# Kernel tuning notes

Hardware: AMD Instinct MI355X
Metric: run time of the kernel (lower is better)

Reference implementation:

```python
import jax, jax.numpy as jnp
import numpy as np

B, N, D = 2, 2048, 1024   # batch, seq_len, d_model
E = 2 * D                  # d_inner = d_model * expand_factor
F = 4 * D                  # ffn hidden
CHUNK = 128
EPS_LN = 1e-5


def setup_inputs() -> dict:
    key = jax.random.key(0)
    ks = jax.random.split(key, 16)
    s = 0.02
    return {
        "x": jax.random.normal(ks[0], (B, N, D), dtype=jnp.float32),
        # linear-attention projections (stored [in, out])
        "q_w": jax.random.normal(ks[1], (D, E), dtype=jnp.float32) * s,
        "q_b": jnp.zeros((E,), jnp.float32),
        "k_w": jax.random.normal(ks[2], (D, E), dtype=jnp.float32) * s,
        "k_b": jnp.zeros((E,), jnp.float32),
        "v_w": jax.random.normal(ks[3], (D, E), dtype=jnp.float32) * s,
        "v_b": jnp.zeros((E,), jnp.float32),
        "o_w": jax.random.normal(ks[4], (E, D), dtype=jnp.float32) * s,
        "o_b": jnp.zeros((D,), jnp.float32),
        # layer norms
        "ln1_g": jnp.ones((D,), jnp.float32), "ln1_b": jnp.zeros((D,), jnp.float32),
        "ln2_g": jnp.ones((D,), jnp.float32), "ln2_b": jnp.zeros((D,), jnp.float32),
        # ffn
        "w1": jax.random.normal(ks[5], (D, F), dtype=jnp.float32) * s,
        "b1": jnp.zeros((F,), jnp.float32),
        "w2": jax.random.normal(ks[6], (F, D), dtype=jnp.float32) * s,
        "b2": jnp.zeros((D,), jnp.float32),
    }


def _layer_norm(x, g, b):
    mu = jnp.mean(x, axis=-1, keepdims=True)
    var = jnp.mean(jnp.square(x - mu), axis=-1, keepdims=True)
    return (x - mu) * jax.lax.rsqrt(var + EPS_LN) * g + b


def _feature_map(x):
    return jax.nn.elu(x) + 1.0  # positive features


def _causal_linear_attention(Q, K, V):
    """Exactly cumsum(k v^T) formulation, computed chunk-recurrently.
    Q,K: [B,N,E] (post feature map), V: [B,N,E]. Returns [B,N,E]."""
    nC = N // CHUNK
    Qc = Q.reshape(B, nC, CHUNK, E).transpose(1, 0, 2, 3)
    Kc = K.reshape(B, nC, CHUNK, E).transpose(1, 0, 2, 3)
    Vc = V.reshape(B, nC, CHUNK, E).transpose(1, 0, 2, 3)
    tril = jnp.tril(jnp.ones((CHUNK, CHUNK), Q.dtype))

    def step(S, qkv):  # S: [B,E,E] running sum of k v^T
        q, k, v = qkv
        scores = jnp.einsum('bcd,bkd->bck', q, k) * tril  # intra-chunk causal
        intra = jnp.einsum('bck,bke->bce', scores, v)
        inter = jnp.einsum('bcd,bde->bce', q, S)
        S = S + jnp.einsum('bcd,bce->bde', k, v)
        return S, intra + inter

    S0 = jnp.zeros((B, E, E), Q.dtype)
    _, num = jax.lax.scan(step, S0, (Qc, Kc, Vc))  # [nC,B,CHUNK,E]
    num = num.transpose(1, 0, 2, 3).reshape(B, N, E)
    Z = jnp.cumsum(K, axis=1)                       # [B,N,E]
    den = jnp.einsum('bnd,bnd->bn', Q, Z)[..., None] + 1e-6
    return num / den


def reference(x, q_w, q_b, k_w, k_b, v_w, v_b, o_w, o_b,
              ln1_g, ln1_b, ln2_g, ln2_b, w1, b1, w2, b2):
    # training branch of SSDFLUIDLayer (linear attention), dropout = identity (eval)
    xn = _layer_norm(x, ln1_g, ln1_b)
    Q = _feature_map(xn @ q_w + q_b)
    K = _feature_map(xn @ k_w + k_b)
    V = xn @ v_w + v_b
    attn = _causal_linear_attention(Q, K, V) @ o_w + o_b
    x = x + attn
    xn2 = _layer_norm(x, ln2_g, ln2_b)
    ffn = jax.nn.gelu(xn2 @ w1 + b1, approximate=False) @ w2 + b2
    return x + ffn
```

## Files before the change

### kernel.cpp

```cpp
#include <hip/hip_runtime.h>
#include <math.h>

typedef unsigned short u16;
typedef short s16x8 __attribute__((ext_vector_type(8)));
typedef float f32x4 __attribute__((ext_vector_type(4)));
typedef long long ll;

__device__ inline u16 f2bf(float f) {
    unsigned u = __float_as_uint(f);
    u += 0x7fffu + ((u >> 16) & 1u);
    return (u16)(u >> 16);
}
__device__ inline float bf2f(u16 h) { return __uint_as_float(((unsigned)h) << 16); }

__device__ __forceinline__ void glds16(const u16* g, u16* l) {
    __builtin_amdgcn_global_load_lds(
        (__attribute__((address_space(1))) void*)(void*)g,
        (__attribute__((address_space(3))) void*)l, 16, 0, 0);
}

__global__ __launch_bounds__(256) void ln_bf16(const float* __restrict__ x,
                                               const float* __restrict__ g,
                                               const float* __restrict__ b,
                                               u16* __restrict__ out, int D) {
    int row = blockIdx.x;
    const float* xr = x + (size_t)row * D;
    int t = threadIdx.x;
    float4 v = ((const float4*)xr)[t];
    float s = v.x + v.y + v.z + v.w;
    __shared__ float sm[4];
    #pragma unroll
    for (int o = 32; o > 0; o >>= 1) s += __shfl_down(s, o, 64);
    int lane = t & 63, wv = t >> 6;
    if (lane == 0) sm[wv] = s;
    __syncthreads();
    float mean = (sm[0] + sm[1] + sm[2] + sm[3]) * (1.0f / 1024.0f);
    float dx = v.x - mean, dy = v.y - mean, dz = v.z - mean, dw = v.w - mean;
    float s2 = dx * dx + dy * dy + dz * dz + dw * dw;
    __syncthreads();
    #pragma unroll
    for (int o = 32; o > 0; o >>= 1) s2 += __shfl_down(s2, o, 64);
    if (lane == 0) sm[wv] = s2;
    __syncthreads();
    float var = (sm[0] + sm[1] + sm[2] + sm[3]) * (1.0f / 1024.0f);
    float rstd = rsqrtf(var + 1e-5f);
    float4 gg = ((const float4*)g)[t], bb = ((const float4*)b)[t];
    ushort4 o4;
    o4.x = f2bf(dx * rstd * gg.x + bb.x);
    o4.y = f2bf(dy * rstd * gg.y + bb.y);
    o4.z = f2bf(dz * rstd * gg.z + bb.z);
    o4.w = f2bf(dw * rstd * gg.w + bb.w);
    ((ushort4*)(out + (size_t)row * D))[t] = o4;
}

__global__ __launch_bounds__(256) void combine_ln(
    const float* __restrict__ x, const float* __restrict__ p0,
    const float* __restrict__ p1, const float* __restrict__ ob,
    const float* __restrict__ g, const float* __restrict__ b,
    float* __restrict__ x2, u16* __restrict__ xn2) {
    int row = blockIdx.x;
    int t = threadIdx.x;
    size_t base = (size_t)row * 256;
    float4 v = ((const float4*)x)[base + t];
    float4 a0 = ((const float4*)p0)[base + t];
    float4 a1 = ((const float4*)p1)[base + t];
    float4 ob4 = ((const float4*)ob)[t];
    v.x += a0.x + a1.x + ob4.x;
    v.y += a0.y + a1.y + ob4.y;
    v.z += a0.z + a1.z + ob4.z;
    v.w += a0.w + a1.w + ob4.w;
    ((float4*)x2)[base + t] = v;
    float s = v.x + v.y + v.z + v.w;
    __shared__ float sm[4];
    #pragma unroll
    for (int o = 32; o > 0; o >>= 1) s += __shfl_down(s, o, 64);
    int lane = t & 63, wv = t >> 6;
    if (lane == 0) sm[wv] = s;
    __syncthreads();
    float mean = (sm[0] + sm[1] + sm[2] + sm[3]) * (1.0f / 1024.0f);
    float dx = v.x - mean, dy = v.y - mean, dz = v.z - mean, dw = v.w - mean;
    float s2 = dx * dx + dy * dy + dz * dz + dw * dw;
    __syncthreads();
    #pragma unroll
    for (int o = 32; o > 0; o >>= 1) s2 += __shfl_down(s2, o, 64);
    if (lane == 0) sm[wv] = s2;
    __syncthreads();
    float var = (sm[0] + sm[1] + sm[2] + sm[3]) * (1.0f / 1024.0f);
    float rstd = rsqrtf(var + 1e-5f);
    float4 gg = ((const float4*)g)[t], bb = ((const float4*)b)[t];
    ushort4 o4;
    o4.x = f2bf(dx * rstd * gg.x + bb.x);
    o4.y = f2bf(dy * rstd * gg.y + bb.y);
    o4.z = f2bf(dz * rstd * gg.z + bb.z);
    o4.w = f2bf(dw * rstd * gg.w + bb.w);
    ((ushort4*)(xn2 + (size_t)row * 1024))[t] = o4;
}

__global__ __launch_bounds__(256) void combine_out(
    const float* __restrict__ x2, const float* __restrict__ p0,
    const float* __restrict__ p1, const float* __restrict__ b2,
    float* __restrict__ out) {
    size_t i = (size_t)blockIdx.x * 256 + threadIdx.x;
    int col4 = (int)(i & 255);
    float4 v = ((const float4*)x2)[i];
    float4 a0 = ((const float4*)p0)[i];
    float4 a1 = ((const float4*)p1)[i];
    float4 bb = ((const float4*)b2)[col4];
    v.x += a0.x + a1.x + bb.x;
    v.y += a0.y + a1.y + bb.y;
    v.z += a0.z + a1.z + bb.z;
    v.w += a0.w + a1.w + bb.w;
    ((float4*)out)[i] = v;
}

__global__ void prep(const float* __restrict__ qb, const float* __restrict__ kb,
                     const float* __restrict__ vb, float* __restrict__ bcat,
                     float* __restrict__ den, int E, int BN) {
    int i = blockIdx.x * 256 + threadIdx.x;
    if (i < E) {
        bcat[i] = qb[i];
        bcat[E + i] = kb[i];
        bcat[2 * E + i] = vb[i];
    }
    if (i < BN) den[i] = 0.f;
}

__global__ __launch_bounds__(256) void transpose_all(
    const float* __restrict__ q_w, const float* __restrict__ k_w,
    const float* __restrict__ v_w, const float* __restrict__ o_w,
    const float* __restrict__ w1, const float* __restrict__ w2,
    u16* __restrict__ qkvT, u16* __restrict__ oT,
    u16* __restrict__ w1T, u16* __restrict__ w2T) {
    int z = blockIdx.y;
    const float* src;
    u16* dst;
    int R, C, tprLog;
    switch (z) {
        case 0: src = q_w; dst = qkvT;                           R = 1024; C = 2048; tprLog = 6; break;
        case 1: src = k_w; dst = qkvT + (size_t)2 * 1024 * 1024; R = 1024; C = 2048; tprLog = 6; break;
        case 2: src = v_w; dst = qkvT + (size_t)4 * 1024 * 1024; R = 1024; C = 2048; tprLog = 6; break;
        case 3: src = o_w; dst = oT;                             R = 2048; C = 1024; tprLog = 5; break;
        case 4: src = w1;  dst = w1T;                            R = 1024; C = 4096; tprLog = 7; break;
        default: src = w2; dst = w2T;                            R = 4096; C = 1024; tprLog = 5; break;
    }
    int bx = blockIdx.x;
    int ntiles = (R >> 5) << (tprLog);
    if (bx >= ntiles) return;
    int c0 = (bx & ((1 << tprLog) - 1)) * 32;
    int r0 = (bx >> tprLog) * 32;
    __shared__ u16 tile[32][33];
    int tx = threadIdx.x & 31, ty = threadIdx.x >> 5;
    #pragma unroll
    for (int i = 0; i < 32; i += 8)
        tile[ty + i][tx] = f2bf(src[(size_t)(r0 + ty + i) * C + c0 + tx]);
    __syncthreads();
    #pragma unroll
    for (int i = 0; i < 32; i += 8)
        dst[(size_t)(c0 + ty + i) * R + r0 + tx] = tile[tx][ty + i];
}

__global__ __launch_bounds__(256) void transpose_u16(const u16* __restrict__ in,
                                                     u16* __restrict__ out,
                                                     int R, int C, int ldIn,
                                                     ll sIn, ll sOut) {
    in += (size_t)blockIdx.z * sIn;
    out += (size_t)blockIdx.z * sOut;
    __shared__ u16 tile[32][33];
    int tx = threadIdx.x & 31, ty = threadIdx.x >> 5;
    int c0 = blockIdx.x * 32, r0 = blockIdx.y * 32;
    #pragma unroll
    for (int i = 0; i < 32; i += 8)
        tile[ty + i][tx] = in[(size_t)(r0 + ty + i) * ldIn + c0 + tx];
    __syncthreads();
    #pragma unroll
    for (int i = 0; i < 32; i += 8)
        out[(size_t)(c0 + ty + i) * R + r0 + tx] = tile[tx][ty + i];
}

enum { EPI_QKV = 0, EPI_TRIL = 2, EPI_DIV = 3, EPI_GELU = 5, EPI_PART = 6 };

template <int EPI, int TNt>
__global__ __launch_bounds__(256, 2) void gemm2b(
    const u16* __restrict__ A, const u16* __restrict__ B, void* __restrict__ Cv,
    const float* __restrict__ bias, float* __restrict__ den,
    int M, int N, int K, int lda, int ldb,
    ll sA, ll sB, ll sC, ll sAux) {

    constexpr int NJ = TNt / 32;
    constexpr int BUF = 4096 + TNt * 32;
    __shared__ __align__(16) u16 lds[3][BUF];

    int z = blockIdx.z;
    A += (size_t)z * sA;
    B += (size_t)z * sB;

    int p = blockIdx.y * gridDim.x + blockIdx.x;
    int m0, n0;
    if (EPI == EPI_TRIL || EPI == EPI_DIV) {
        int nb = gridDim.x;
        int panel = nb * 4;
        int pp = p / panel, rr2 = p - pp * panel;
        m0 = (pp * 4 + (rr2 & 3)) * 128;
        n0 = (rr2 >> 2) * TNt;
    } else {
        int g = p & 7, rr2 = p >> 3;
        int lw = gridDim.x >> 2, lh = gridDim.y >> 1;
        int ly = rr2 / lw, lx = rr2 - ly * lw;
        m0 = ((g >> 2) * lh + ly) * 128;
        n0 = ((g & 3) * lw + lx) * TNt;
    }

    int t = threadIdx.x;

    if (EPI == EPI_TRIL && n0 > m0 + 127) {
        u16* C = (u16*)Cv + (size_t)z * sC;
        #pragma unroll
        for (int s = 0; s < 8; ++s) {
            int v = t + 256 * s;
            int row = v >> 4, cf = (v & 15) * 8;
            *(uint4*)&C[(size_t)(m0 + row) * N + n0 + cf] = make_uint4(0, 0, 0, 0);
        }
        return;
    }

    int lane = t & 63, wid = t >> 6;
    int lr = lane & 15, q = lane >> 4;

    int skf = (((lane & 3) - ((lane >> 3) & 3)) & 3) * 8;
    const u16* gA = A + (size_t)(m0 + wid * 32 + (lane >> 2)) * lda + skf;
    const u16* gB = B + (size_t)(n0 + wid * (TNt / 4) + (lane >> 2)) * ldb + skf;
    int sdA = wid * 1024;
    int sdB = 4096 + wid * (TNt * 32 / 4);

    int kend = (EPI == EPI_DIV) ? (m0 + 128 < K ? m0 + 128 : K) : K;
    int nk = kend >> 5;

    auto stageA = [&](int tt, int d) {
        int kt = (tt < nk ? tt : nk - 1) << 5;
        glds16(gA + kt, &lds[d][sdA]);
        glds16(gA + kt + (size_t)16 * lda, &lds[d][sdA + 512]);
    };
    auto stageB = [&](int tt, int d) {
        int kt = (tt < nk ? tt : nk - 1) << 5;
        #pragma unroll
        for (int r2 = 0; r2 < TNt / 64; ++r2)
            glds16(gB + kt + (size_t)(16 * r2) * ldb, &lds[d][sdB + r2 * 512]);
    };

    f32x4 acc[4][NJ];
    #pragma unroll
    for (int i = 0; i < 4; i++)
        #pragma unroll
        for (int j = 0; j < NJ; j++) { f32x4 zz = {0.f, 0.f, 0.f, 0.f}; acc[i][j] = zz; }

    int wm = (wid & 1) * 64, wn = (wid >> 1) * (TNt / 2);
    int csw = ((q + (lr >> 1)) & 3) * 8;
    int aoff = (wm + lr) * 32 + csw;
    int boff = 4096 + (wn + lr) * 32 + csw;

    stageA(0, 0); stageB(0, 0);
    stageA(1, 1); stageB(1, 1);
    if constexpr (TNt == 256) asm volatile("s_waitcnt vmcnt(6)" ::: "memory");
    else                      asm volatile("s_waitcnt vmcnt(4)" ::: "memory");
    asm volatile("s_barrier" ::: "memory");

    s16x8 af[4], bf_[NJ];

    int cur = 0;
    for (int tt = 0; tt < nk; ++tt) {
        int nx2 = cur + 2; if (nx2 >= 3) nx2 -= 3;
        const u16* L = &lds[cur][0];

        #pragma unroll
        for (int j = 0; j < NJ / 2; j++) bf_[j] = *(const s16x8*)&L[boff + j * 512];
        #pragma unroll
        for (int i = 0; i < 4; i++) af[i] = *(const s16x8*)&L[aoff + i * 512];
        stageB(tt + 2, nx2);
        asm volatile("s_barrier" ::: "memory");
        __builtin_amdgcn_s_setprio(1);
        #pragma unroll
        for (int i = 0; i < 4; i++)
            #pragma unroll
            for (int j = 0; j < NJ / 2; j++)
                acc[i][j] = __builtin_amdgcn_mfma_f32_16x16x32_bf16(af[i], bf_[j], acc[i][j], 0, 0, 0);
        __builtin_amdgcn_s_setprio(0);
        asm volatile("s_barrier" ::: "memory");

        #pragma unroll
        for (int j = NJ / 2; j < NJ; j++) bf_[j] = *(const s16x8*)&L[boff + j * 512];
        stageA(tt + 2, nx2);
        asm volatile("s_barrier" ::: "memory");
        __builtin_amdgcn_s_setprio(1);
        #pragma unroll
        for (int i = 0; i < 4; i++)
            #pragma unroll
            for (int j = NJ / 2; j < NJ; j++)
                acc[i][j] = __builtin_amdgcn_mfma_f32_16x16x32_bf16(af[i], bf_[j], acc[i][j], 0, 0, 0);
        __builtin_amdgcn_s_setprio(0);
        if constexpr (TNt == 256) asm volatile("s_waitcnt vmcnt(6)" ::: "memory");
        else                      asm volatile("s_waitcnt vmcnt(4)" ::: "memory");
        asm volatile("s_barrier" ::: "memory");

        cur = cur + 1; if (cur >= 3) cur -= 3;
    }

    asm volatile("s_waitcnt vmcnt(0)" ::: "memory");

    u16* Cb = (u16*)Cv + (size_t)z * ((EPI == EPI_PART) ? 0 : sC);
    float* Cf = (float*)Cv + (size_t)z * ((EPI == EPI_PART) ? sC : 0);
    bool isQKcol = (EPI == EPI_QKV);
    #pragma unroll
    for (int i = 0; i < 4; i++) {
        #pragma unroll
        for (int r = 0; r < 4; r++) {
            int row = m0 + wm + i * 16 + q * 4 + r;
            float rs = 0.f;
            #pragma unroll
            for (int j = 0; j < NJ; j++) {
                int col = n0 + wn + j * 16 + lr;
                float v = acc[i][j][r];
                if (EPI == EPI_PART) {
                    Cf[(size_t)row * N + col] = v;
                } else if (EPI == EPI_TRIL) {
                    v = (col <= row) ? v : 0.f;
                    rs += v;
                    Cb[(size_t)row * N + col] = f2bf(v);
                } else if (EPI == EPI_DIV) {
                    float d = den[(size_t)z * sAux + row] + 1e-6f;
                    Cb[(size_t)row * N + col] = f2bf(v / d);
                } else {
                    v += bias[col];
                    if (EPI == EPI_QKV) {
                        if (isQKcol && (n0 + wn + j * 16 < 4096)) v = (v > 0.f) ? (v + 1.f) : __expf(v);
                    } else {
                        float u = v * (0.7978845608f + 0.0356774081f * v * v);
                        u = fminf(u, 40.f);
                        float e = __expf(2.f * u);
                        v = v * __fdividef(e, e + 1.f);
                    }
                    Cb[(size_t)row * N + col] = f2bf(v);
                }
            }
            if (EPI == EPI_TRIL) {
                #pragma unroll
                for (int m = 1; m < 16; m <<= 1) rs += __shfl_xor(rs, m, 16);
                if (lr == 0) atomicAdd(&den[(size_t)z * sAux + row], rs);
            }
        }
    }
}

extern "C" void kernel_launch(void* const* d_in, const int* in_sizes, int n_in,
                              void* d_out, int out_size, void* d_ws, size_t ws_size,
                              hipStream_t stream) {
    const float* x    = (const float*)d_in[0];
    const float* q_w  = (const float*)d_in[1];
    const float* q_b  = (const float*)d_in[2];
    const float* k_w  = (const float*)d_in[3];
    const float* k_b  = (const float*)d_in[4];
    const float* v_w  = (const float*)d_in[5];
    const float* v_b  = (const float*)d_in[6];
    const float* o_w  = (const float*)d_in[7];
    const float* o_b  = (const float*)d_in[8];
    const float* ln1g = (const float*)d_in[9];
    const float* ln1b = (const float*)d_in[10];
    const float* ln2g = (const float*)d_in[11];
    const float* ln2b = (const float*)d_in[12];
    const float* w1   = (const float*)d_in[13];
    const float* b1   = (const float*)d_in[14];
    const float* w2   = (const float*)d_in[15];
    const float* b2   = (const float*)d_in[16];
    float* out = (float*)d_out;

    constexpr int Bb = 2, N = 2048, D = 1024, E = 2048, F = 4096;
    constexpr int BN = Bb * N;
    constexpr int E3 = 3 * E;

    char* ws = (char*)d_ws;
    size_t off = 0;
    auto alloc = [&](size_t bytes) -> void* {
        void* p = ws + off;
        off += (bytes + 255) & ~(size_t)255;
        return p;
    };
    u16*   qkvT = (u16*)alloc((size_t)E3 * D * 2);
    u16*   oT   = (u16*)alloc((size_t)D * E * 2);
    u16*   w1T  = (u16*)alloc((size_t)F * D * 2);
    u16*   w2T  = (u16*)alloc((size_t)D * F * 2);
    float* bcat = (float*)alloc((size_t)E3 * 4);
    u16*   xn   = (u16*)alloc((size_t)BN * D * 2);
    u16*   QKV  = (u16*)alloc((size_t)BN * E3 * 2);
    u16*   Vt   = (u16*)alloc((size_t)Bb * E * N * 2);
    u16*   Amat = (u16*)alloc((size_t)Bb * N * N * 2);
    float* den  = (float*)alloc((size_t)BN * 4);

    u16*   xn2 = xn;
    u16*   P   = QKV;
    u16*   h   = QKV + (size_t)8 * 1024 * 1024;
    float* x2  = (float*)Vt;
    float* pt0 = (float*)Amat;
    float* pt1 = pt0 + (size_t)BN * D;

    dim3 blk(256);

    prep<<<dim3((BN + 255) / 256), blk, 0, stream>>>(q_b, k_b, v_b, bcat, den, E, BN);

    transpose_all<<<dim3(4096, 6), blk, 0, stream>>>(
        q_w, k_w, v_w, o_w, w1, w2, qkvT, oT, w1T, w2T);

    ln_bf16<<<BN, blk, 0, stream>>>(x, ln1g, ln1b, xn, D);

    gemm2b<EPI_QKV, 256><<<dim3(E3 / 256, BN / 128), blk, 0, stream>>>(
        xn, qkvT, QKV, bcat, nullptr, BN, E3, D, D, D, 0, 0, 0, 0);

    transpose_u16<<<dim3(E / 32, N / 32, Bb), blk, 0, stream>>>(
        QKV + 2 * E, Vt, N, E, E3, (ll)N * E3, (ll)E * N);

    gemm2b<EPI_TRIL, 128><<<dim3(N / 128, N / 128, Bb), blk, 0, stream>>>(
        QKV, QKV + E, Amat, nullptr, den, N, N, E, E3, E3,
        (ll)N * E3, (ll)N * E3, (ll)N * N, (ll)N);

    gemm2b<EPI_DIV, 128><<<dim3(E / 128, N / 128, Bb), blk, 0, stream>>>(
        Amat, Vt, P, nullptr, den, N, E, N, N, N,
        (ll)N * N, (ll)E * N, (ll)N * E, (ll)N);

    gemm2b<EPI_PART, 128><<<dim3(D / 128, BN / 128, 2), blk, 0, stream>>>(
        P, oT, pt0, nullptr, nullptr, BN, D, E / 2, E, E,
        (ll)(E / 2), (ll)(E / 2), (ll)BN * D, 0);

    combine_ln<<<BN, blk, 0, stream>>>(x, pt0, pt1, o_b, ln2g, ln2b, x2, xn2);

    gemm2b<EPI_GELU, 256><<<dim3(F / 256, BN / 128), blk, 0, stream>>>(
        xn2, w1T, h, b1, nullptr, BN, F, D, D, D, 0, 0, 0, 0);

    gemm2b<EPI_PART, 128><<<dim3(D / 128, BN / 128, 2), blk, 0, stream>>>(
        h, w2T, pt0, nullptr, nullptr, BN, D, F / 2, F, F,
        (ll)(F / 2), (ll)(F / 2), (ll)BN * D, 0);

    combine_out<<<dim3(BN * D / 4 / 256), blk, 0, stream>>>(x2, pt0, pt1, b2, out);
}
```

Measured before the change: 442.3 us.

## Fuse preprocessing kernels and write transposed V directly from QKV GEMM epilogue

Merges the bias/den init, weight transpose and first layer-norm into one preproc launch, using an extra grid slice for the layernorm rows. The QKV GEMM epilogue now transposes V tiles through LDS and writes Vt directly, so the separate transpose_u16 kernel and the V columns of QKV are no longer written or read. This removes three launches and a round trip through global memory. In exchange the epilogue is more complex, and the V-tile blocks do extra LDS traffic and synchronisation.

```diff
diff --git a/kernel.cpp b/kernel.cpp
--- a/kernel.cpp
+++ b/kernel.cpp
@@ -11,7 +11,6 @@
     u += 0x7fffu + ((u >> 16) & 1u);
     return (u16)(u >> 16);
 }
-__device__ inline float bf2f(u16 h) { return __uint_as_float(((unsigned)h) << 16); }
 
 __device__ __forceinline__ void glds16(const u16* g, u16* l) {
     __builtin_amdgcn_global_load_lds(
@@ -19,38 +18,79 @@
         (__attribute__((address_space(3))) void*)l, 16, 0, 0);
 }
 
-__global__ __launch_bounds__(256) void ln_bf16(const float* __restrict__ x,
-                                               const float* __restrict__ g,
-                                               const float* __restrict__ b,
-                                               u16* __restrict__ out, int D) {
-    int row = blockIdx.x;
-    const float* xr = x + (size_t)row * D;
+__global__ __launch_bounds__(256) void preproc(
+    const float* __restrict__ q_w, const float* __restrict__ k_w,
+    const float* __restrict__ v_w, const float* __restrict__ o_w,
+    const float* __restrict__ w1, const float* __restrict__ w2,
+    u16* __restrict__ qkvT, u16* __restrict__ oT,
+    u16* __restrict__ w1T, u16* __restrict__ w2T,
+    const float* __restrict__ x, const float* __restrict__ g,
+    const float* __restrict__ b, u16* __restrict__ xn,
+    const float* __restrict__ qb, const float* __restrict__ kb,
+    const float* __restrict__ vb, float* __restrict__ bcat,
+    float* __restrict__ den) {
+    __shared__ u16 tile[32][33];
+    __shared__ float sm[4];
+    int z = blockIdx.y;
     int t = threadIdx.x;
-    float4 v = ((const float4*)xr)[t];
-    float s = v.x + v.y + v.z + v.w;
-    __shared__ float sm[4];
-    #pragma unroll
-    for (int o = 32; o > 0; o >>= 1) s += __shfl_down(s, o, 64);
-    int lane = t & 63, wv = t >> 6;
-    if (lane == 0) sm[wv] = s;
+
+    if (z == 6) {
+        int row = blockIdx.x;
+        int i = row * 256 + t;
+        if (i < 2048) { bcat[i] = qb[i]; bcat[2048 + i] = kb[i]; bcat[4096 + i] = vb[i]; }
+        if (i < 4096) den[i] = 0.f;
+        const float* xr = x + (size_t)row * 1024;
+        float4 v = ((const float4*)xr)[t];
+        float s = v.x + v.y + v.z + v.w;
+        #pragma unroll
+        for (int o = 32; o > 0; o >>= 1) s += __shfl_down(s, o, 64);
+        int lane = t & 63, wv = t >> 6;
+        if (lane == 0) sm[wv] = s;
+        __syncthreads();
+        float mean = (sm[0] + sm[1] + sm[2] + sm[3]) * (1.0f / 1024.0f);
+        float dx = v.x - mean, dy = v.y - mean, dz = v.z - mean, dw = v.w - mean;
+        float s2 = dx * dx + dy * dy + dz * dz + dw * dw;
+        __syncthreads();
+        #pragma unroll
+        for (int o = 32; o > 0; o >>= 1) s2 += __shfl_down(s2, o, 64);
+        if (lane == 0) sm[wv] = s2;
+        __syncthreads();
+        float var = (sm[0] + sm[1] + sm[2] + sm[3]) * (1.0f / 1024.0f);
+        float rstd = rsqrtf(var + 1e-5f);
+        float4 gg = ((const float4*)g)[t], bb = ((const float4*)b)[t];
+        ushort4 o4;
+        o4.x = f2bf(dx * rstd * gg.x + bb.x);
+        o4.y = f2bf(dy * rstd * gg.y + bb.y);
+        o4.z = f2bf(dz * rstd * gg.z + bb.z);
+        o4.w = f2bf(dw * rstd * gg.w + bb.w);
+        ((ushort4*)(xn + (size_t)row * 1024))[t] = o4;
+        return;
+    }
+
+    const float* src;
+    u16* dst;
+    int R, C, tprLog;
+    switch (z) {
+        case 0: src = q_w; dst = qkvT;                           R = 1024; C = 2048; tprLog = 6; break;
+        case 1: src = k_w; dst = qkvT + (size_t)2 * 1024 * 1024; R = 1024; C = 2048; tprLog = 6; break;
+        case 2: src = v_w; dst = qkvT + (size_t)4 * 1024 * 1024; R = 1024; C = 2048; tprLog = 6; break;
+        case 3: src = o_w; dst = oT;                             R = 2048; C = 1024; tprLog = 5; break;
+        case 4: src = w1;  dst = w1T;                            R = 1024; C = 4096; tprLog = 7; break;
+        default: src = w2; dst = w2T;                            R = 4096; C = 1024; tprLog = 5; break;
+    }
+    int bx = blockIdx.x;
+    int ntiles = (R >> 5) << (tprLog);
+    if (bx >= ntiles) return;
+    int c0 = (bx & ((1 << tprLog) - 1)) * 32;
+    int r0 = (bx >> tprLog) * 32;
+    int tx = t & 31, ty = t >> 5;
+    #pragma unroll
+    for (int i = 0; i < 32; i += 8)
+        tile[ty + i][tx] = f2bf(src[(size_t)(r0 + ty + i) * C + c0 + tx]);
     __syncthreads();
-    float mean = (sm[0] + sm[1] + sm[2] + sm[3]) * (1.0f / 1024.0f);
-    float dx = v.x - mean, dy = v.y - mean, dz = v.z - mean, dw = v.w - mean;
-    float s2 = dx * dx + dy * dy + dz * dz + dw * dw;
-    __syncthreads();
-    #pragma unroll
-    for (int o = 32; o > 0; o >>= 1) s2 += __shfl_down(s2, o, 64);
-    if (lane == 0) sm[wv] = s2;
-    __syncthreads();
-    float var = (sm[0] + sm[1] + sm[2] + sm[3]) * (1.0f / 1024.0f);
-    float rstd = rsqrtf(var + 1e-5f);
-    float4 gg = ((const float4*)g)[t], bb = ((const float4*)b)[t];
-    ushort4 o4;
-    o4.x = f2bf(dx * rstd * gg.x + bb.x);
-    o4.y = f2bf(dy * rstd * gg.y + bb.y);
-    o4.z = f2bf(dz * rstd * gg.z + bb.z);
-    o4.w = f2bf(dw * rstd * gg.w + bb.w);
-    ((ushort4*)(out + (size_t)row * D))[t] = o4;
+    #pragma unroll
+    for (int i = 0; i < 32; i += 8)
+        dst[(size_t)(c0 + ty + i) * R + r0 + tx] = tile[tx][ty + i];
 }
 
 __global__ __launch_bounds__(256) void combine_ln(
@@ -113,76 +153,12 @@
     ((float4*)out)[i] = v;
 }
 
-__global__ void prep(const float* __restrict__ qb, const float* __restrict__ kb,
-                     const float* __restrict__ vb, float* __restrict__ bcat,
-                     float* __restrict__ den, int E, int BN) {
-    int i = blockIdx.x * 256 + threadIdx.x;
-    if (i < E) {
-        bcat[i] = qb[i];
-        bcat[E + i] = kb[i];
-        bcat[2 * E + i] = vb[i];
-    }
-    if (i < BN) den[i] = 0.f;
-}
-
-__global__ __launch_bounds__(256) void transpose_all(
-    const float* __restrict__ q_w, const float* __restrict__ k_w,
-    const float* __restrict__ v_w, const float* __restrict__ o_w,
-    const float* __restrict__ w1, const float* __restrict__ w2,
-    u16* __restrict__ qkvT, u16* __restrict__ oT,
-    u16* __restrict__ w1T, u16* __restrict__ w2T) {
-    int z = blockIdx.y;
-    const float* src;
-    u16* dst;
-    int R, C, tprLog;
-    switch (z) {
-        case 0: src = q_w; dst = qkvT;                           R = 1024; C = 2048; tprLog = 6; break;
-        case 1: src = k_w; dst = qkvT + (size_t)2 * 1024 * 1024; R = 1024; C = 2048; tprLog = 6; break;
-        case 2: src = v_w; dst = qkvT + (size_t)4 * 1024 * 1024; R = 1024; C = 2048; tprLog = 6; break;
-        case 3: src = o_w; dst = oT;                             R = 2048; C = 1024; tprLog = 5; break;
-        case 4: src = w1;  dst = w1T;                            R = 1024; C = 4096; tprLog = 7; break;
-        default: src = w2; dst = w2T;                            R = 4096; C = 1024; tprLog = 5; break;
-    }
-    int bx = blockIdx.x;
-    int ntiles = (R >> 5) << (tprLog);
-    if (bx >= ntiles) return;
-    int c0 = (bx & ((1 << tprLog) - 1)) * 32;
-    int r0 = (bx >> tprLog) * 32;
-    __shared__ u16 tile[32][33];
-    int tx = threadIdx.x & 31, ty = threadIdx.x >> 5;
-    #pragma unroll
-    for (int i = 0; i < 32; i += 8)
-        tile[ty + i][tx] = f2bf(src[(size_t)(r0 + ty + i) * C + c0 + tx]);
-    __syncthreads();
-    #pragma unroll
-    for (int i = 0; i < 32; i += 8)
-        dst[(size_t)(c0 + ty + i) * R + r0 + tx] = tile[tx][ty + i];
-}
-
-__global__ __launch_bounds__(256) void transpose_u16(const u16* __restrict__ in,
-                                                     u16* __restrict__ out,
-                                                     int R, int C, int ldIn,
-                                                     ll sIn, ll sOut) {
-    in += (size_t)blockIdx.z * sIn;
-    out += (size_t)blockIdx.z * sOut;
-    __shared__ u16 tile[32][33];
-    int tx = threadIdx.x & 31, ty = threadIdx.x >> 5;
-    int c0 = blockIdx.x * 32, r0 = blockIdx.y * 32;
-    #pragma unroll
-    for (int i = 0; i < 32; i += 8)
-        tile[ty + i][tx] = in[(size_t)(r0 + ty + i) * ldIn + c0 + tx];
-    __syncthreads();
-    #pragma unroll
-    for (int i = 0; i < 32; i += 8)
-        out[(size_t)(c0 + ty + i) * R + r0 + tx] = tile[tx][ty + i];
-}
-
 enum { EPI_QKV = 0, EPI_TRIL = 2, EPI_DIV = 3, EPI_GELU = 5, EPI_PART = 6 };
 
 template <int EPI, int TNt>
 __global__ __launch_bounds__(256, 2) void gemm2b(
     const u16* __restrict__ A, const u16* __restrict__ B, void* __restrict__ Cv,
-    const float* __restrict__ bias, float* __restrict__ den,
+    const float* __restrict__ bias, float* __restrict__ den, u16* __restrict__ aux,
     int M, int N, int K, int lda, int ldb,
     ll sA, ll sB, ll sC, ll sAux) {
 
@@ -306,9 +282,37 @@
 
     asm volatile("s_waitcnt vmcnt(0)" ::: "memory");
 
+    if constexpr (EPI == EPI_QKV) {
+        if (n0 >= 4096) {
+            __syncthreads();
+            u16* Lb = (u16*)&lds[0][0];
+            #pragma unroll
+            for (int i = 0; i < 4; i++)
+                #pragma unroll
+                for (int r = 0; r < 4; r++) {
+                    int rl = wm + i * 16 + q * 4 + r;
+                    #pragma unroll
+                    for (int j = 0; j < NJ; j++) {
+                        int cl = wn + j * 16 + lr;
+                        float v = acc[i][j][r] + bias[n0 + cl];
+                        Lb[cl * 136 + rl] = f2bf(v);
+                    }
+                }
+            __syncthreads();
+            int b_ = m0 >> 11, nloc = m0 & 2047;
+            u16* vt = aux + (size_t)b_ * 2048 * 2048 + (size_t)(n0 - 4096) * 2048 + nloc;
+            int ec = t >> 4, nc = (t & 15) * 8;
+            #pragma unroll
+            for (int it = 0; it < 16; ++it) {
+                int e = ec + it * 16;
+                *(s16x8*)&vt[(size_t)e * 2048 + nc] = *(const s16x8*)&Lb[e * 136 + nc];
+            }
+            return;
+        }
+    }
+
     u16* Cb = (u16*)Cv + (size_t)z * ((EPI == EPI_PART) ? 0 : sC);
     float* Cf = (float*)Cv + (size_t)z * ((EPI == EPI_PART) ? sC : 0);
-    bool isQKcol = (EPI == EPI_QKV);
     #pragma unroll
     for (int i = 0; i < 4; i++) {
         #pragma unroll
@@ -331,7 +335,7 @@
                 } else {
                     v += bias[col];
                     if (EPI == EPI_QKV) {
-                        if (isQKcol && (n0 + wn + j * 16 < 4096)) v = (v > 0.f) ? (v + 1.f) : __expf(v);
+                        v = (v > 0.f) ? (v + 1.f) : __expf(v);
                     } else {
                         float u = v * (0.7978845608f + 0.0356774081f * v * v);
                         u = fminf(u, 40.f);
@@ -403,38 +407,32 @@
 
     dim3 blk(256);
 
-    prep<<<dim3((BN + 255) / 256), blk, 0, stream>>>(q_b, k_b, v_b, bcat, den, E, BN);
-
-    transpose_all<<<dim3(4096, 6), blk, 0, stream>>>(
-        q_w, k_w, v_w, o_w, w1, w2, qkvT, oT, w1T, w2T);
-
-    ln_bf16<<<BN, blk, 0, stream>>>(x, ln1g, ln1b, xn, D);
+    preproc<<<dim3(4096, 7), blk, 0, stream>>>(
+        q_w, k_w, v_w, o_w, w1, w2, qkvT, oT, w1T, w2T,
+        x, ln1g, ln1b, xn, q_b, k_b, v_b, bcat, den);
 
     gemm2b<EPI_QKV, 256><<<dim3(E3 / 256, BN / 128), blk, 0, stream>>>(
-        xn, qkvT, QKV, bcat, nullptr, BN, E3, D, D, D, 0, 0, 0, 0);
-
-    transpose_u16<<<dim3(E / 32, N / 32, Bb), blk, 0, stream>>>(
-        QKV + 2 * E, Vt, N, E, E3, (ll)N * E3, (ll)E * N);
+        xn, qkvT, QKV, bcat, nullptr, Vt, BN, E3, D, D, D, 0, 0, 0, 0);
 
     gemm2b<EPI_TRIL, 128><<<dim3(N / 128, N / 128, Bb), blk, 0, stream>>>(
-        QKV, QKV + E, Amat, nullptr, den, N, N, E, E3, E3,
+        QKV, QKV + E, Amat, nullptr, den, nullptr, N, N, E, E3, E3,
         (ll)N * E3, (ll)N * E3, (ll)N * N, (ll)N);
 
     gemm2b<EPI_DIV, 128><<<dim3(E / 128, N / 128, Bb), blk, 0, stream>>>(
-        Amat, Vt, P, nullptr, den, N, E, N, N, N,
+        Amat, Vt, P, nullptr, den, nullptr, N, E, N, N, N,
         (ll)N * N, (ll)E * N, (ll)N * E, (ll)N);
 
     gemm2b<EPI_PART, 128><<<dim3(D / 128, BN / 128, 2), blk, 0, stream>>>(
-        P, oT, pt0, nullptr, nullptr, BN, D, E / 2, E, E,
+        P, oT, pt0, nullptr, nullptr, nullptr, BN, D, E / 2, E, E,
         (ll)(E / 2), (ll)(E / 2), (ll)BN * D, 0);
 
     combine_ln<<<BN, blk, 0, stream>>>(x, pt0, pt1, o_b, ln2g, ln2b, x2, xn2);
 
     gemm2b<EPI_GELU, 256><<<dim3(F / 256, BN / 128), blk, 0, stream>>>(
-        xn2, w1T, h, b1, nullptr, BN, F, D, D, D, 0, 0, 0, 0);
+        xn2, w1T, h, b1, nullptr, nullptr, BN, F, D, D, D, 0, 0, 0, 0);
 
     gemm2b<EPI_PART, 128><<<dim3(D / 128, BN / 128, 2), blk, 0, stream>>>(
-        h, w2T, pt0, nullptr, nullptr, BN, D, F / 2, F, F,
+        h, w2T, pt0, nullptr, nullptr, nullptr, BN, D, F / 2, F, F,
         (ll)(F / 2), (ll)(F / 2), (ll)BN * D, 0);
 
     combine_out<<<dim3(BN * D / 4 / 256), blk, 0, stream>>>(x2, pt0, pt1, b2, out);
```

After: 427.0 us. -3.5%, faster.
